# Kernel tuning notes

Hardware: AMD Instinct MI355X
Metric: run time of the kernel (lower is better)

## Reference

```python
import jax, jax.numpy as jnp
import numpy as np
from jax import lax

N_G, E_G, E_LG = 100000, 400000, 1200000
N_T, E_T, E_LGT = 50000, 100000, 300000
D_F, D_MSG_G = 64, 128
VOCAB, D_EMB, D_MSG_T = 780, 128, 128
N_ITERS_G, N_ITERS_T = 4, 4
SCALE = 0.05  # keep relu/sum chains numerically tame over iterations


def setup_inputs() -> dict:
    key = jax.random.key(0)
    ks = jax.random.split(key, 32)
    f32 = jnp.float32
    w = lambda k, sh: jax.random.normal(k, sh, f32) * SCALE
    return {
        "G_f": jax.random.normal(ks[0], (N_G, D_F), f32),
        "G_ef": jax.random.normal(ks[1], (E_G, D_F), f32),
        "G_src": jax.random.randint(ks[2], (E_G,), 0, N_G, jnp.int32),
        "G_dst": jax.random.randint(ks[3], (E_G,), 0, N_G, jnp.int32),
        "G_lg_src": jax.random.randint(ks[4], (E_LG,), 0, E_G, jnp.int32),
        "G_lg_dst": jax.random.randint(ks[5], (E_LG,), 0, E_G, jnp.int32),
        "T_id": jax.random.randint(ks[6], (N_T,), 0, VOCAB, jnp.int32),
        "T_src": jax.random.randint(ks[7], (E_T,), 0, N_T, jnp.int32),
        "T_dst": jax.random.randint(ks[8], (E_T,), 0, N_T, jnp.int32),
        "T_lg_src": jax.random.randint(ks[9], (E_LGT,), 0, E_T, jnp.int32),
        "T_lg_dst": jax.random.randint(ks[10], (E_LGT,), 0, E_T, jnp.int32),
        "embeddings": jax.random.normal(ks[11], (VOCAB, D_EMB), f32),
        "W1": w(ks[12], (D_F, D_MSG_G)),
        "W2": w(ks[13], (D_F, D_MSG_G)),
        "W3": w(ks[14], (D_MSG_G, D_MSG_G)),
        "U1_G": w(ks[15], (D_F, D_MSG_G)),
        "U2_G": w(ks[16], (D_MSG_G, D_MSG_G)),
        "Wz": w(ks[17], (D_EMB, D_MSG_T)),
        "Uz": w(ks[18], (D_MSG_T, D_MSG_T)),
        "Wr": w(ks[19], (D_EMB, D_MSG_T)),
        "Ur": w(ks[20], (D_MSG_T, D_MSG_T)),
        "Wh": w(ks[21], (D_EMB, D_MSG_T)),
        "Uh": w(ks[22], (D_MSG_T, D_MSG_T)),
        "U1_T": w(ks[23], (D_EMB, D_MSG_T)),
        "U2_T": w(ks[24], (D_MSG_T, D_MSG_T)),
    }


def reference(G_f, G_ef, G_src, G_dst, G_lg_src, G_lg_dst,
              T_id, T_src, T_dst, T_lg_src, T_lg_dst,
              embeddings, W1, W2, W3, U1_G, U2_G,
              Wz, Uz, Wr, Ur, Wh, Uh, U1_T, U2_T):
    seg = jax.ops.segment_sum

    # ---- molecule graph G: loopy-BP MLP messages on the line graph ----
    f_src_G = G_f[G_src]                               # [E_G, D_F] copy_src
    base_G = f_src_G @ W1 + G_ef @ W2                  # loop-invariant part of g1_G

    def stepG(msg, _):
        sum_msg = seg(msg[G_lg_src], G_lg_dst, num_segments=E_G)
        return jax.nn.relu(base_G + sum_msg @ W3), None

    msgG0 = jnp.zeros((E_G, D_MSG_G), G_f.dtype)
    msgG, _ = lax.scan(stepG, msgG0, None, length=N_ITERS_G)

    # readout g2_G: sum edge msgs into dst nodes
    sG = seg(msgG, G_dst, num_segments=N_G)
    x_G = jax.nn.relu(G_f @ U1_G + sG @ U2_G)          # [N_G, D_MSG_G]

    # ---- junction tree T: GRU messages on the tree line graph ----
    f_T = embeddings[T_id]                             # one-hot id @ embeddings
    f_src_T = f_T[T_src]                               # [E_T, D_EMB]
    xz, xr, xh = f_src_T @ Wz, f_src_T @ Wr, f_src_T @ Wh

    def stepT(msg, _):
        s = seg(msg[T_lg_src], T_lg_dst, num_segments=E_T)
        z = jax.nn.sigmoid(xz + s @ Uz)
        r = jax.nn.sigmoid(xr + s @ Ur)
        h = jnp.tanh(xh + (r * s) @ Uh)
        return (1.0 - z) * s + z * h, None

    msgT0 = jnp.zeros((E_T, D_MSG_T), f_T.dtype)
    msgT, _ = lax.scan(stepT, msgT0, None, length=N_ITERS_T)

    sT = seg(msgT, T_dst, num_segments=N_T)
    x_T = jax.nn.relu(f_T @ U1_T + sT @ U2_T)          # [N_T, D_MSG_T]

    # concat node readouts (same width) so output is a single array
    return jnp.concatenate([x_G, x_T], axis=0)         # [N_G+N_T, 128]
```

## Files before the change

### kernel.cpp

```cpp
#include <hip/hip_runtime.h>

#define NG 100000
#define EG 400000
#define ELG 1200000
#define NT 50000
#define ET 100000
#define ELGT 300000

#define GEG ((EG + 63) / 64)
#define GET ((ET + 63) / 64)
#define GNG ((NG + 63) / 64)
#define GNT ((NT + 63) / 64)

#define SEG1 EG
#define SEG2 (EG + NG)
#define SEG3 (EG + NG + ET)
#define NSEG_ALL (EG + NG + ET + NT)
#define NE_ALL (ELG + EG + ELGT + ET)

typedef unsigned short u16;
typedef unsigned int u32;
typedef __attribute__((ext_vector_type(8))) short bf16x8;
typedef __attribute__((ext_vector_type(4))) float f32x4;

#define TILE_B 16384

__device__ __forceinline__ float bflo(u32 p){ return __uint_as_float(p << 16); }
__device__ __forceinline__ float bfhi(u32 p){ return __uint_as_float(p & 0xffff0000u); }
__device__ __forceinline__ float bf2f(u16 h){ return __uint_as_float(((u32)h) << 16); }
__device__ __forceinline__ u16 f2bf(float f){
  u32 u = __float_as_uint(f);
  u32 r = u + 0x7fffu + ((u >> 16) & 1u);
  return (u16)(r >> 16);
}
__device__ __forceinline__ float sigm(float x){ return 1.0f / (1.0f + __expf(-x)); }
__device__ __forceinline__ float tanh_(float x){ return 2.0f / (1.0f + __expf(-2.0f * x)) - 1.0f; }
__device__ __forceinline__ float relu_(float x){ return x > 0.0f ? x : 0.0f; }
__device__ __forceinline__ void wfence(){ __builtin_amdgcn_wave_barrier(); }

__device__ __forceinline__ int swz(int r, int c){ return r * 256 + (c ^ ((r & 7) << 4)); }

__device__ __forceinline__ void zero8(float v[8]){
  #pragma unroll
  for (int j = 0; j < 8; j++) v[j] = 0.f;
}
__device__ __forceinline__ uint4 pack8(const float v[8]){
  uint4 o;
  o.x = f2bf(v[0]) | ((u32)f2bf(v[1]) << 16);
  o.y = f2bf(v[2]) | ((u32)f2bf(v[3]) << 16);
  o.z = f2bf(v[4]) | ((u32)f2bf(v[5]) << 16);
  o.w = f2bf(v[6]) | ((u32)f2bf(v[7]) << 16);
  return o;
}
__device__ __forceinline__ uint2 pack4(const f32x4& a){
  uint2 o;
  o.x = (u32)f2bf(a[0]) | ((u32)f2bf(a[1]) << 16);
  o.y = (u32)f2bf(a[2]) | ((u32)f2bf(a[3]) << 16);
  return o;
}
__device__ __forceinline__ uint2 pack4a(const float v[4]){
  uint2 o;
  o.x = (u32)f2bf(v[0]) | ((u32)f2bf(v[1]) << 16);
  o.y = (u32)f2bf(v[2]) | ((u32)f2bf(v[3]) << 16);
  return o;
}
__device__ __forceinline__ void unp4(uint2 u, float v[4]){
  v[0] = bflo(u.x); v[1] = bfhi(u.x); v[2] = bflo(u.y); v[3] = bfhi(u.y);
}
__device__ __forceinline__ bf16x8 packfrag(const float v[8]){
  union { uint4 u; bf16x8 b; } c; c.u = pack8(v); return c.b;
}
__device__ __forceinline__ bf16x8 zfrag(){
  union { uint4 u; bf16x8 b; } c; c.u = make_uint4(0, 0, 0, 0); return c.b;
}
__device__ __forceinline__ bf16x8 as_frag(uint4 u){
  union { uint4 u; bf16x8 b; } c; c.u = u; return c.b;
}

__global__ void k_sniff(const u32* __restrict__ g, int* __restrict__ flag){
  __shared__ int sh[2];
  if (threadIdx.x < 2) sh[threadIdx.x] = 0;
  __syncthreads();
  int c0 = 0, c1 = 0;
  for (int i = 0; i < 16; i++){
    u32 w = g[threadIdx.x * 16 + i];
    u32 lo = w & 0xFFFFu;
    if (lo == 0u) c0++;
    else { u32 e = (lo >> 7) & 0xFFu; if (e >= 96u && e <= 144u) c1++; }
  }
  atomicAdd(&sh[0], c0); atomicAdd(&sh[1], c1);
  __syncthreads();
  if (threadIdx.x == 0) *flag = (sh[0] < 512 && sh[1] > 2048) ? 1 : 0;
}

__global__ void k_cvt_all(const void* p0, const void* p1, const void* p2, const void* p3,
                          const void* p4, const void* p5, const void* p6, const void* p7,
                          const void* p8, const void* p9, const void* p10, const void* p11,
                          const void* p12, float* __restrict__ wm, const int* __restrict__ flagp){
  int i = blockIdx.x * 256 + threadIdx.x;
  if (i >= 188416) return;
  const int offs[14] = {0,8192,16384,32768,40960,57344,73728,90112,106496,122880,139264,155648,172032,188416};
  const void* ps[13] = {p0,p1,p2,p3,p4,p5,p6,p7,p8,p9,p10,p11,p12};
  int w = 0;
  while (i >= offs[w + 1]) w++;
  int li = i - offs[w];
  wm[i] = (*flagp) ? bf2f(((const u16*)ps[w])[li]) : ((const float*)ps[w])[li];
}

__global__ void k_mkfrag_all(const float* __restrict__ wm, u16* __restrict__ frag){
  const int wmo[13] = {0,8192,16384,32768,40960,57344,73728,90112,106496,122880,139264,155648,172032};
  const int nks[13] = {2,2,4,2,4,4,4,4,4,4,4,4,4};
  int b = blockIdx.x;
  int wi = 0, ks = b;
  while (ks >= nks[wi]){ ks -= nks[wi]; wi++; }
  const float* W = wm + wmo[wi];
  int nt = threadIdx.x >> 6, lane = threadIdx.x & 63;
  int kr = ks * 32 + ((lane >> 4) << 3);
  int col = nt * 16 + (lane & 15);
  u16* o = frag + (size_t)b * 4096 + nt * 512 + lane * 8;
  #pragma unroll
  for (int j = 0; j < 8; j++) o[j] = f2bf(W[(size_t)(kr + j) * 128 + col]);
}

__device__ __forceinline__ const void* rowdt(const void* mat, size_t row, int W, int bf){
  return bf ? (const void*)((const u16*)mat + row * (size_t)W)
            : (const void*)((const float*)mat + row * (size_t)W);
}
__device__ __forceinline__ void load8(const void* rowbase, int c8, int bf, float v[8]){
  if (bf){
    uint4 d = ((const uint4*)rowbase)[c8];
    v[0]=bflo(d.x); v[1]=bfhi(d.x); v[2]=bflo(d.y); v[3]=bfhi(d.y);
    v[4]=bflo(d.z); v[5]=bfhi(d.z); v[6]=bflo(d.w); v[7]=bfhi(d.w);
  } else {
    const float4* p = (const float4*)rowbase + (c8 << 1);
    float4 a = p[0], b = p[1];
    v[0]=a.x; v[1]=a.y; v[2]=a.z; v[3]=a.w; v[4]=b.x; v[5]=b.y; v[6]=b.z; v[7]=b.w;
  }
}

__global__ void k_hist_all(const int* __restrict__ Glgd, const int* __restrict__ Gd,
                           const int* __restrict__ Tlgd, const int* __restrict__ Td,
                           int* __restrict__ cnt){
  int e = blockIdx.x * 256 + threadIdx.x;
  if (e >= NE_ALL) return;
  int seg;
  if (e < ELG)                       seg = Glgd[e];
  else if (e < ELG + EG)             seg = SEG1 + Gd[e - ELG];
  else if (e < ELG + EG + ELGT)      seg = SEG2 + Tlgd[e - ELG - EG];
  else                               seg = SEG3 + Td[e - ELG - EG - ELGT];
  atomicAdd(&cnt[seg], 1);
}

__global__ void k_scan1(const int* __restrict__ cnt, int n, int* __restrict__ csum){
  int base = blockIdx.x * 4096, tid = threadIdx.x;
  int s = 0;
  for (int i = 0; i < 16; i++){ int idx = base + i * 256 + tid; if (idx < n) s += cnt[idx]; }
  __shared__ int red[4];
  for (int off = 32; off; off >>= 1) s += __shfl_down(s, off, 64);
  if ((tid & 63) == 0) red[tid >> 6] = s;
  __syncthreads();
  if (tid == 0) csum[blockIdx.x] = red[0] + red[1] + red[2] + red[3];
}

__global__ void k_scan2(int* csum, int nch, int* rowptr, int n){
  if (threadIdx.x == 0){
    int run = 0;
    for (int c = 0; c < nch; c++){ int t = csum[c]; csum[c] = run; run += t; }
    rowptr[n] = run;
  }
}

__global__ void k_scan3(const int* __restrict__ cnt, int n, const int* __restrict__ csum,
                        int* __restrict__ rowptr){
  __shared__ int buf[4096];
  __shared__ int tsum[256];
  int base = blockIdx.x * 4096, tid = threadIdx.x;
  for (int i = 0; i < 16; i++){ int idx = base + i * 256 + tid; buf[i * 256 + tid] = (idx < n) ? cnt[idx] : 0; }
  __syncthreads();
  int run = 0;
  for (int i = 0; i < 16; i++){ int v = buf[tid * 16 + i]; buf[tid * 16 + i] = run; run += v; }
  tsum[tid] = run;
  __syncthreads();
  for (int off = 1; off < 256; off <<= 1){
    int v = (tid >= off) ? tsum[tid - off] : 0;
    __syncthreads();
    tsum[tid] += v;
    __syncthreads();
  }
  int texcl = tsum[tid] - run;
  int cbase = csum[blockIdx.x];
  for (int i = 0; i < 16; i++){
    int idx = base + tid * 16 + i;
    if (idx < n) rowptr[idx] = cbase + texcl + buf[tid * 16 + i];
  }
}

__global__ void k_fill_all(const int* __restrict__ Glgd, const int* __restrict__ Glgs,
                           const int* __restrict__ Gd,
                           const int* __restrict__ Tlgd, const int* __restrict__ Tlgs,
                           const int* __restrict__ Td,
                           const int* __restrict__ rowptr, int* __restrict__ fill,
                           int* __restrict__ col){
  int e = blockIdx.x * 256 + threadIdx.x;
  if (e >= NE_ALL) return;
  int seg, srcv;
  if (e < ELG){                      seg = Glgd[e];                           srcv = Glgs[e]; }
  else if (e < ELG + EG){            int l = e - ELG;                         seg = SEG1 + Gd[l];   srcv = l; }
  else if (e < ELG + EG + ELGT){     int l = e - ELG - EG;                    seg = SEG2 + Tlgd[l]; srcv = Tlgs[l]; }
  else {                             int l = e - ELG - EG - ELGT;             seg = SEG3 + Td[l];   srcv = l; }
  int pos = atomicAdd(&fill[seg], 1);
  col[rowptr[seg] + pos] = srcv;
}


__device__ __forceinline__ void acc8_add(float (&a)[8], uint4 d){
  a[0] += bflo(d.x); a[1] += bfhi(d.x);
  a[2] += bflo(d.y); a[3] += bfhi(d.y);
  a[4] += bflo(d.z); a[5] += bfhi(d.z);
  a[6] += bflo(d.w); a[7] += bfhi(d.w);
}

__device__ __forceinline__ void gather_accum(const int* __restrict__ rowptr,
    const int* __restrict__ colidx, const u16* __restrict__ msg,
    int row, int M, int kg, float (&acc)[4][8])
{
  #pragma unroll
  for (int ks = 0; ks < 4; ks++) zero8(acc[ks]);
  if (row >= M) return;
  int p = rowptr[row], pe = rowptr[row + 1];
  for (; p + 1 < pe; p += 2){
    const uint4* b0 = (const uint4*)(msg + (size_t)colidx[p] * 128);
    const uint4* b1 = (const uint4*)(msg + (size_t)colidx[p + 1] * 128);
    uint4 v0[4], v1[4];
    #pragma unroll
    for (int ks = 0; ks < 4; ks++){ v0[ks] = b0[ks * 4 + kg]; v1[ks] = b1[ks * 4 + kg]; }
    #pragma unroll
    for (int ks = 0; ks < 4; ks++){ acc8_add(acc[ks], v0[ks]); acc8_add(acc[ks], v1[ks]); }
  }
  if (p < pe){
    const uint4* b0 = (const uint4*)(msg + (size_t)colidx[p] * 128);
    #pragma unroll
    for (int ks = 0; ks < 4; ks++){ uint4 v = b0[ks * 4 + kg]; acc8_add(acc[ks], v); }
  }
}

template<int KS>
__device__ __forceinline__ void mma_f(const bf16x8* a, const u16* __restrict__ frag,
                                      f32x4 (&acc)[8])
{
  int lane = threadIdx.x & 63;
  #pragma unroll
  for (int ks = 0; ks < KS; ks++){
    const u16* fb = frag + (size_t)ks * 4096 + lane * 8;
    #pragma unroll
    for (int nt = 0; nt < 8; nt++){
      bf16x8 b = *(const bf16x8*)(fb + (size_t)nt * 512);
      acc[nt] = __builtin_amdgcn_mfma_f32_16x16x32_bf16(a[ks], b, acc[nt], 0, 0, 0);
    }
  }
}

#define INIT_ACC(A) { _Pragma("unroll") for (int n_=0;n_<8;n_++){ A[n_][0]=0.f; A[n_][1]=0.f; A[n_][2]=0.f; A[n_][3]=0.f; } }

__device__ __forceinline__ void repack_store(const char* __restrict__ tile,
    u16* __restrict__ dst, int row0, int M)
{
  int rl = threadIdx.x >> 2, q = threadIdx.x & 3;
  int grow = row0 + rl;
  if (grow < M){
    #pragma unroll
    for (int v = 0; v < 4; v++){
      uint4 d = *(const uint4*)(tile + swz(rl, (v * 4 + q) * 16));
      *(uint4*)(dst + (size_t)grow * 128 + (size_t)(v * 4 + q) * 8) = d;
    }
  }
}

__device__ __forceinline__ size_t fslot(int blk, int w, int nt){
  return ((((size_t)blk * 4 + w) * 8 + nt) * 64 + (threadIdx.x & 63)) * 4;
}

__device__ __forceinline__ void load_catfrag(const void* __restrict__ Gf,
    const void* __restrict__ Gef, const int* __restrict__ Gsrc,
    int arow, int kg, int bf, bf16x8 (&fC)[4])
{
  if (arow < EG){
    int sr = Gsrc[arow];
    const void* ra = rowdt(Gf, (size_t)sr, 64, bf);
    const void* rb = rowdt(Gef, (size_t)arow, 64, bf);
    float t[8];
    load8(ra, kg, bf, t);     fC[0] = packfrag(t);
    load8(ra, 4 + kg, bf, t); fC[1] = packfrag(t);
    load8(rb, kg, bf, t);     fC[2] = packfrag(t);
    load8(rb, 4 + kg, bf, t); fC[3] = packfrag(t);
  } else {
    #pragma unroll
    for (int ks = 0; ks < 4; ks++) fC[ks] = zfrag();
  }
}


__global__ __launch_bounds__(256) void k_init(
    const void* __restrict__ Gf, const void* __restrict__ Gef, const int* __restrict__ Gsrc,
    const u16* __restrict__ fWcat, const int* __restrict__ flagp, u16* __restrict__ msgG,
    const void* __restrict__ emb, const int* __restrict__ Tid, const int* __restrict__ Tsrc,
    const u16* __restrict__ fWz, const u16* __restrict__ fWr, const u16* __restrict__ fWh,
    u16* __restrict__ xzf, u16* __restrict__ xrf, u16* __restrict__ xhf, u16* __restrict__ msgT)
{
  __shared__ char t0[TILE_B];
  int bf = *flagp;
  int lane = threadIdx.x & 63, w = threadIdx.x >> 6;
  int stripe = w * 16, kg = lane >> 4, m16 = lane & 15;
  if (blockIdx.x < GET){
    int blk = blockIdx.x, row0 = blk * 64, arow = row0 + stripe + m16;
    bf16x8 fE[4];
    if (arow < ET){
      int id = Tid[Tsrc[arow]];
      const void* rb = rowdt(emb, (size_t)id, 128, bf);
      #pragma unroll
      for (int ks = 0; ks < 4; ks++){
        float t[8]; load8(rb, ks * 4 + kg, bf, t); fE[ks] = packfrag(t);
      }
    } else {
      #pragma unroll
      for (int ks = 0; ks < 4; ks++) fE[ks] = zfrag();
    }
    f32x4 aZ[8], aR[8]; INIT_ACC(aZ); INIT_ACC(aR);
    mma_f<4>(fE, fWz, aZ);
    mma_f<4>(fE, fWr, aR);
    #pragma unroll
    for (int nt = 0; nt < 8; nt++){
      *(uint2*)(xzf + fslot(blk, w, nt)) = pack4(aZ[nt]);
      *(uint2*)(xrf + fslot(blk, w, nt)) = pack4(aR[nt]);
    }
    f32x4 aH[8]; INIT_ACC(aH);
    mma_f<4>(fE, fWh, aH);
    #pragma unroll
    for (int nt = 0; nt < 8; nt++){
      *(uint2*)(xhf + fslot(blk, w, nt)) = pack4(aH[nt]);
      #pragma unroll
      for (int r = 0; r < 4; r++){
        int rt = stripe + (kg << 2) + r;
        int cb = nt * 32 + m16 * 2;
        *(u16*)(t0 + swz(rt, cb)) = f2bf(sigm(aZ[nt][r]) * tanh_(aH[nt][r]));
      }
    }
    wfence();
    repack_store(t0, msgT, row0, ET);
  } else {
    int blk = blockIdx.x - GET, row0 = blk * 64, arow = row0 + stripe + m16;
    bf16x8 fC[4];
    load_catfrag(Gf, Gef, Gsrc, arow, kg, bf, fC);
    f32x4 acc[8]; INIT_ACC(acc);
    mma_f<4>(fC, fWcat, acc);
    #pragma unroll
    for (int nt = 0; nt < 8; nt++)
      #pragma unroll
      for (int r = 0; r < 4; r++){
        int rt = stripe + (kg << 2) + r;
        int cb = nt * 32 + m16 * 2;
        *(u16*)(t0 + swz(rt, cb)) = f2bf(relu_(acc[nt][r]));
      }
    wfence();
    repack_store(t0, msgG, row0, EG);
  }
}

__global__ __launch_bounds__(256) void k_iter(
    const u16* __restrict__ msgInG, u16* __restrict__ msgOutG,
    const void* __restrict__ Gf, const void* __restrict__ Gef, const int* __restrict__ Gsrc,
    const int* __restrict__ rp, const int* __restrict__ col,
    const u16* __restrict__ fWcat, const u16* __restrict__ fW3, const int* __restrict__ flagp,
    const u16* __restrict__ msgInT, u16* __restrict__ msgOutT,
    const u16* __restrict__ fUz, const u16* __restrict__ fUr, const u16* __restrict__ fUh,
    const u16* __restrict__ xzf, const u16* __restrict__ xrf, const u16* __restrict__ xhf)
{
  __shared__ char t0[TILE_B];
  int lane = threadIdx.x & 63, w = threadIdx.x >> 6;
  int stripe = w * 16, kg = lane >> 4, m16 = lane & 15;
  if (blockIdx.x < GET){
    int blk = blockIdx.x, row0 = blk * 64, arow = row0 + stripe + m16;
    float ga[4][8];
    gather_accum(rp + SEG2, col, msgInT, arow, ET, kg, ga);
    bf16x8 fS[4];
    #pragma unroll
    for (int ks = 0; ks < 4; ks++){
      uint4 pk = pack8(ga[ks]);
      *(uint4*)(t0 + swz(stripe + m16, ks * 64 + kg * 16)) = pk;
      fS[ks] = as_frag(pk);
    }
    f32x4 aZ[8], aR[8]; INIT_ACC(aZ); INIT_ACC(aR);
    mma_f<4>(fS, fUz, aZ);
    mma_f<4>(fS, fUr, aR);
    wfence();
    uint2 zpk[8], wpk[8];
    #pragma unroll
    for (int nt = 0; nt < 8; nt++){
      uint2 z4 = *(const uint2*)(xzf + fslot(blk, w, nt));
      uint2 r4 = *(const uint2*)(xrf + fslot(blk, w, nt));
      float xzv[4], xrv[4], zv[4], wv[4];
      unp4(z4, xzv); unp4(r4, xrv);
      #pragma unroll
      for (int r = 0; r < 4; r++){
        int rt = stripe + (kg << 2) + r;
        int cb = nt * 32 + m16 * 2;
        float s = bf2f(*(const u16*)(t0 + swz(rt, cb)));
        float z = sigm(xzv[r] + aZ[nt][r]);
        float rr = sigm(xrv[r] + aR[nt][r]);
        zv[r] = z;
        wv[r] = s * (1.f - z);
        *(u16*)(t0 + swz(rt, cb)) = f2bf(rr * s);
      }
      zpk[nt] = pack4a(zv); wpk[nt] = pack4a(wv);
    }
    wfence();
    bf16x8 fRS[4];
    #pragma unroll
    for (int ks = 0; ks < 4; ks++)
      fRS[ks] = *(const bf16x8*)(t0 + swz(stripe + m16, ks * 64 + kg * 16));
    f32x4 aH[8]; INIT_ACC(aH);
    mma_f<4>(fRS, fUh, aH);
    wfence();
    #pragma unroll
    for (int nt = 0; nt < 8; nt++){
      uint2 h4 = *(const uint2*)(xhf + fslot(blk, w, nt));
      float xhv[4], zv[4], wv[4];
      unp4(h4, xhv); unp4(zpk[nt], zv); unp4(wpk[nt], wv);
      #pragma unroll
      for (int r = 0; r < 4; r++){
        float h = tanh_(xhv[r] + aH[nt][r]);
        float m = wv[r] + zv[r] * h;
        int rt = stripe + (kg << 2) + r;
        int cb = nt * 32 + m16 * 2;
        *(u16*)(t0 + swz(rt, cb)) = f2bf(m);
      }
    }
    wfence();
    repack_store(t0, msgOutT, row0, ET);
  } else {
    int bf = *flagp;
    int blk = blockIdx.x - GET, row0 = blk * 64, arow = row0 + stripe + m16;
    bf16x8 fC[4];
    load_catfrag(Gf, Gef, Gsrc, arow, kg, bf, fC);
    float ga[4][8];
    gather_accum(rp, col, msgInG, arow, EG, kg, ga);
    bf16x8 fS[4];
    #pragma unroll
    for (int ks = 0; ks < 4; ks++) fS[ks] = packfrag(ga[ks]);
    f32x4 acc[8]; INIT_ACC(acc);
    mma_f<4>(fS, fW3, acc);
    mma_f<4>(fC, fWcat, acc);
    #pragma unroll
    for (int nt = 0; nt < 8; nt++)
      #pragma unroll
      for (int r = 0; r < 4; r++){
        int rt = stripe + (kg << 2) + r;
        int cb = nt * 32 + m16 * 2;
        *(u16*)(t0 + swz(rt, cb)) = f2bf(relu_(acc[nt][r]));
      }
    wfence();
    repack_store(t0, msgOutG, row0, EG);
  }
}

__global__ __launch_bounds__(256) void k_readout(
    const void* __restrict__ Gf, const u16* __restrict__ msgG,
    const int* __restrict__ rp, const int* __restrict__ col,
    const u16* __restrict__ fU1G, const u16* __restrict__ fU2G,
    const void* __restrict__ emb, const int* __restrict__ Tid, const u16* __restrict__ msgT,
    const u16* __restrict__ fU1T, const u16* __restrict__ fU2T,
    const int* __restrict__ flagp, float* __restrict__ out)
{
  int bf = *flagp;
  int lane = threadIdx.x & 63, w = threadIdx.x >> 6;
  int stripe = w * 16, kg = lane >> 4, m16 = lane & 15;
  if (blockIdx.x < GNT){
    int row0 = blockIdx.x * 64, arow = row0 + stripe + m16;
    bf16x8 fE[4];
    if (arow < NT){
      int id = Tid[arow];
      const void* rb = rowdt(emb, (size_t)id, 128, bf);
      #pragma unroll
      for (int ks = 0; ks < 4; ks++){
        float t[8]; load8(rb, ks * 4 + kg, bf, t); fE[ks] = packfrag(t);
      }
    } else {
      #pragma unroll
      for (int ks = 0; ks < 4; ks++) fE[ks] = zfrag();
    }
    float ga[4][8];
    gather_accum(rp + SEG3, col, msgT, arow, NT, kg, ga);
    bf16x8 fS[4];
    #pragma unroll
    for (int ks = 0; ks < 4; ks++) fS[ks] = packfrag(ga[ks]);
    f32x4 acc[8]; INIT_ACC(acc);
    mma_f<4>(fE, fU1T, acc);
    mma_f<4>(fS, fU2T, acc);
    #pragma unroll
    for (int nt = 0; nt < 8; nt++)
      #pragma unroll
      for (int r = 0; r < 4; r++){
        int R = row0 + stripe + (kg << 2) + r;
        if (R < NT) out[(size_t)(NG + R) * 128 + nt * 16 + m16] = relu_(acc[nt][r]);
      }
  } else {
    int row0 = (blockIdx.x - GNT) * 64, arow = row0 + stripe + m16;
    bf16x8 fG[2];
    if (arow < NG){
      const void* ra = rowdt(Gf, (size_t)arow, 64, bf);
      float t[8];
      load8(ra, kg, bf, t);     fG[0] = packfrag(t);
      load8(ra, 4 + kg, bf, t); fG[1] = packfrag(t);
    } else { fG[0] = zfrag(); fG[1] = zfrag(); }
    float ga[4][8];
    gather_accum(rp + SEG1, col, msgG, arow, NG, kg, ga);
    bf16x8 fS[4];
    #pragma unroll
    for (int ks = 0; ks < 4; ks++) fS[ks] = packfrag(ga[ks]);
    f32x4 acc[8]; INIT_ACC(acc);
    mma_f<2>(fG, fU1G, acc);
    mma_f<4>(fS, fU2G, acc);
    #pragma unroll
    for (int nt = 0; nt < 8; nt++)
      #pragma unroll
      for (int r = 0; r < 4; r++){
        int R = row0 + stripe + (kg << 2) + r;
        if (R < NG) out[(size_t)R * 128 + nt * 16 + m16] = relu_(acc[nt][r]);
      }
  }
}

extern "C" void kernel_launch(void* const* d_in, const int* in_sizes, int n_in,
                              void* d_out, int out_size, void* d_ws, size_t ws_size,
                              hipStream_t stream)
{
  const void* G_f      = d_in[0];
  const void* G_ef     = d_in[1];
  const int*  G_src    = (const int*)d_in[2];
  const int*  G_dst    = (const int*)d_in[3];
  const int*  G_lg_src = (const int*)d_in[4];
  const int*  G_lg_dst = (const int*)d_in[5];
  const int*  T_id     = (const int*)d_in[6];
  const int*  T_src    = (const int*)d_in[7];
  const int*  T_dst    = (const int*)d_in[8];
  const int*  T_lg_src = (const int*)d_in[9];
  const int*  T_lg_dst = (const int*)d_in[10];
  const void* emb      = d_in[11];
  float* out = (float*)d_out;
  (void)in_sizes; (void)n_in; (void)out_size; (void)ws_size;

  size_t off = 0;
  auto alloc = [&](size_t bytes) -> char* {
    char* p = (char*)d_ws + off;
    off += (bytes + 255) & ~(size_t)255;
    return p;
  };

  int*   flag = (int*)alloc(256);
  float* wm   = (float*)alloc(sizeof(float) * 188416);
  u16*   frag = (u16*)alloc(2 * 46 * 4096);
  const u16* fWcat = frag;
  const u16* fW3   = frag + (size_t)4  * 4096;
  const u16* fU1G  = frag + (size_t)8  * 4096;
  const u16* fU2G  = frag + (size_t)10 * 4096;
  const u16* fWz   = frag + (size_t)14 * 4096;
  const u16* fUz   = frag + (size_t)18 * 4096;
  const u16* fWr   = frag + (size_t)22 * 4096;
  const u16* fUr   = frag + (size_t)26 * 4096;
  const u16* fWh   = frag + (size_t)30 * 4096;
  const u16* fUh   = frag + (size_t)34 * 4096;
  const u16* fU1T  = frag + (size_t)38 * 4096;
  const u16* fU2T  = frag + (size_t)42 * 4096;

  int* rp   = (int*)alloc(sizeof(int) * (NSEG_ALL + 1));
  int* col  = (int*)alloc(sizeof(int) * NE_ALL);
  int* cnt  = (int*)alloc(sizeof(int) * 2 * NSEG_ALL);
  int* csum = (int*)alloc(sizeof(int) * 256);
  u16* msgGA = (u16*)alloc((size_t)EG * 128 * 2);
  u16* msgGB = (u16*)alloc((size_t)EG * 128 * 2);
  u16* xzf   = (u16*)alloc((size_t)GET * 8192 * 2);
  u16* xrf   = (u16*)alloc((size_t)GET * 8192 * 2);
  u16* xhf   = (u16*)alloc((size_t)GET * 8192 * 2);
  u16* msgTA = (u16*)alloc((size_t)ET * 128 * 2);
  u16* msgTB = (u16*)alloc((size_t)ET * 128 * 2);

  k_sniff<<<1, 256, 0, stream>>>((const u32*)G_ef, flag);
  k_cvt_all<<<(188416 + 255) / 256, 256, 0, stream>>>(
      d_in[12], d_in[13], d_in[14], d_in[15], d_in[16], d_in[17], d_in[18],
      d_in[19], d_in[20], d_in[21], d_in[22], d_in[23], d_in[24], wm, flag);
  k_mkfrag_all<<<46, 512, 0, stream>>>(wm, frag);

  hipMemsetAsync(cnt, 0, sizeof(int) * 2 * NSEG_ALL, stream);
  k_hist_all<<<(NE_ALL + 255) / 256, 256, 0, stream>>>(G_lg_dst, G_dst, T_lg_dst, T_dst, cnt);
  int nch = (NSEG_ALL + 4095) / 4096;
  k_scan1<<<nch, 256, 0, stream>>>(cnt, NSEG_ALL, csum);
  k_scan2<<<1, 64, 0, stream>>>(csum, nch, rp, NSEG_ALL);
  k_scan3<<<nch, 256, 0, stream>>>(cnt, NSEG_ALL, csum, rp);
  k_fill_all<<<(NE_ALL + 255) / 256, 256, 0, stream>>>(
      G_lg_dst, G_lg_src, G_dst, T_lg_dst, T_lg_src, T_dst, rp, cnt + NSEG_ALL, col);

  k_init<<<GET + GEG, 256, 0, stream>>>(G_f, G_ef, G_src, fWcat, flag, msgGA,
                                        emb, T_id, T_src, fWz, fWr, fWh, xzf, xrf, xhf, msgTA);
  k_iter<<<GET + GEG, 256, 0, stream>>>(msgGA, msgGB, G_f, G_ef, G_src, rp, col, fWcat, fW3, flag,
                                        msgTA, msgTB, fUz, fUr, fUh, xzf, xrf, xhf);
  k_iter<<<GET + GEG, 256, 0, stream>>>(msgGB, msgGA, G_f, G_ef, G_src, rp, col, fWcat, fW3, flag,
                                        msgTB, msgTA, fUz, fUr, fUh, xzf, xrf, xhf);
  k_iter<<<GET + GEG, 256, 0, stream>>>(msgGA, msgGB, G_f, G_ef, G_src, rp, col, fWcat, fW3, flag,
                                        msgTA, msgTB, fUz, fUr, fUh, xzf, xrf, xhf);
  k_readout<<<GNT + GNG, 256, 0, stream>>>(G_f, msgGB, rp, col, fU1G, fU2G,
                                           emb, T_id, msgTB, fU1T, fU2T, flag, out);
}
```

Before: 1.246 ms.

## Pad CSR rows to multiples of four and cut register pressure in GRU kernels

CSR rows are padded to multiples of four and filled with a dummy index that points at an extra zeroed message row, so the gather loop always loads four neighbour rows per step with no tail branch. The GRU step is reordered to compute r, then h, then z, using a second LDS tile so fewer accumulator arrays are live at once. k_init, k_iter and k_readout get launch bounds that request higher occupancy, and in the G branch of k_iter and in k_readout the gathers are moved ahead of the other loads. This trades extra padded loads of a zero row and added LDS use for more memory-level parallelism and occupancy; the tighter register limit may cause spills.

```diff
diff --git a/kernel.cpp b/kernel.cpp
--- a/kernel.cpp
+++ b/kernel.cpp
@@ -17,6 +17,7 @@
 #define SEG3 (EG + NG + ET)
 #define NSEG_ALL (EG + NG + ET + NT)
 #define NE_ALL (ELG + EG + ELGT + ET)
+#define NE_PAD (NE_ALL + 3 * NSEG_ALL + 64)
 
 typedef unsigned short u16;
 typedef unsigned int u32;
@@ -56,12 +57,6 @@
   uint2 o;
   o.x = (u32)f2bf(a[0]) | ((u32)f2bf(a[1]) << 16);
   o.y = (u32)f2bf(a[2]) | ((u32)f2bf(a[3]) << 16);
-  return o;
-}
-__device__ __forceinline__ uint2 pack4a(const float v[4]){
-  uint2 o;
-  o.x = (u32)f2bf(v[0]) | ((u32)f2bf(v[1]) << 16);
-  o.y = (u32)f2bf(v[2]) | ((u32)f2bf(v[3]) << 16);
   return o;
 }
 __device__ __forceinline__ void unp4(uint2 u, float v[4]){
@@ -154,7 +149,10 @@
 __global__ void k_scan1(const int* __restrict__ cnt, int n, int* __restrict__ csum){
   int base = blockIdx.x * 4096, tid = threadIdx.x;
   int s = 0;
-  for (int i = 0; i < 16; i++){ int idx = base + i * 256 + tid; if (idx < n) s += cnt[idx]; }
+  for (int i = 0; i < 16; i++){
+    int idx = base + i * 256 + tid;
+    if (idx < n) s += (cnt[idx] + 3) & ~3;
+  }
   __shared__ int red[4];
   for (int off = 32; off; off >>= 1) s += __shfl_down(s, off, 64);
   if ((tid & 63) == 0) red[tid >> 6] = s;
@@ -175,7 +173,10 @@
   __shared__ int buf[4096];
   __shared__ int tsum[256];
   int base = blockIdx.x * 4096, tid = threadIdx.x;
-  for (int i = 0; i < 16; i++){ int idx = base + i * 256 + tid; buf[i * 256 + tid] = (idx < n) ? cnt[idx] : 0; }
+  for (int i = 0; i < 16; i++){
+    int idx = base + i * 256 + tid;
+    buf[i * 256 + tid] = (idx < n) ? ((cnt[idx] + 3) & ~3) : 0;
+  }
   __syncthreads();
   int run = 0;
   for (int i = 0; i < 16; i++){ int v = buf[tid * 16 + i]; buf[tid * 16 + i] = run; run += v; }
@@ -212,6 +213,24 @@
   col[rowptr[seg] + pos] = srcv;
 }
 
+__global__ void k_fill_pad(const int* __restrict__ cnt, const int* __restrict__ rowptr,
+                           int* __restrict__ col){
+  int seg = blockIdx.x * 256 + threadIdx.x;
+  if (seg >= NSEG_ALL) return;
+  int dummy = (seg < SEG2) ? EG : ET;
+  int start = rowptr[seg] + cnt[seg];
+  int end = rowptr[seg + 1];
+  for (int q = start; q < end; q++) col[q] = dummy;
+}
+
+__global__ void k_zero_dummy(u16* a, u16* b, u16* c, u16* d){
+  int i = threadIdx.x;
+  if (i < 128){
+    a[(size_t)EG * 128 + i] = 0; b[(size_t)EG * 128 + i] = 0;
+    c[(size_t)ET * 128 + i] = 0; d[(size_t)ET * 128 + i] = 0;
+  }
+}
+
 
 __device__ __forceinline__ void acc8_add(float (&a)[8], uint4 d){
   a[0] += bflo(d.x); a[1] += bfhi(d.x);
@@ -228,19 +247,23 @@
   for (int ks = 0; ks < 4; ks++) zero8(acc[ks]);
   if (row >= M) return;
   int p = rowptr[row], pe = rowptr[row + 1];
-  for (; p + 1 < pe; p += 2){
-    const uint4* b0 = (const uint4*)(msg + (size_t)colidx[p] * 128);
-    const uint4* b1 = (const uint4*)(msg + (size_t)colidx[p + 1] * 128);
-    uint4 v0[4], v1[4];
-    #pragma unroll
-    for (int ks = 0; ks < 4; ks++){ v0[ks] = b0[ks * 4 + kg]; v1[ks] = b1[ks * 4 + kg]; }
-    #pragma unroll
-    for (int ks = 0; ks < 4; ks++){ acc8_add(acc[ks], v0[ks]); acc8_add(acc[ks], v1[ks]); }
-  }
-  if (p < pe){
-    const uint4* b0 = (const uint4*)(msg + (size_t)colidx[p] * 128);
-    #pragma unroll
-    for (int ks = 0; ks < 4; ks++){ uint4 v = b0[ks * 4 + kg]; acc8_add(acc[ks], v); }
+  for (; p < pe; p += 4){
+    int i0 = colidx[p], i1 = colidx[p + 1], i2 = colidx[p + 2], i3 = colidx[p + 3];
+    const uint4* b0 = (const uint4*)(msg + (size_t)i0 * 128);
+    const uint4* b1 = (const uint4*)(msg + (size_t)i1 * 128);
+    const uint4* b2 = (const uint4*)(msg + (size_t)i2 * 128);
+    const uint4* b3 = (const uint4*)(msg + (size_t)i3 * 128);
+    uint4 v0[4], v1[4], v2[4], v3[4];
+    #pragma unroll
+    for (int ks = 0; ks < 4; ks++){
+      v0[ks] = b0[ks * 4 + kg]; v1[ks] = b1[ks * 4 + kg];
+      v2[ks] = b2[ks * 4 + kg]; v3[ks] = b3[ks * 4 + kg];
+    }
+    #pragma unroll
+    for (int ks = 0; ks < 4; ks++){
+      acc8_add(acc[ks], v0[ks]); acc8_add(acc[ks], v1[ks]);
+      acc8_add(acc[ks], v2[ks]); acc8_add(acc[ks], v3[ks]);
+    }
   }
 }
 
@@ -300,7 +323,7 @@
 }
 
 
-__global__ __launch_bounds__(256) void k_init(
+__global__ __launch_bounds__(256, 4) void k_init(
     const void* __restrict__ Gf, const void* __restrict__ Gef, const int* __restrict__ Gsrc,
     const u16* __restrict__ fWcat, const int* __restrict__ flagp, u16* __restrict__ msgG,
     const void* __restrict__ emb, const int* __restrict__ Tid, const int* __restrict__ Tsrc,
@@ -325,24 +348,31 @@
       #pragma unroll
       for (int ks = 0; ks < 4; ks++) fE[ks] = zfrag();
     }
-    f32x4 aZ[8], aR[8]; INIT_ACC(aZ); INIT_ACC(aR);
-    mma_f<4>(fE, fWz, aZ);
-    mma_f<4>(fE, fWr, aR);
+    f32x4 acc[8];
+    uint2 zpk[8];
+    INIT_ACC(acc);
+    mma_f<4>(fE, fWz, acc);
     #pragma unroll
     for (int nt = 0; nt < 8; nt++){
-      *(uint2*)(xzf + fslot(blk, w, nt)) = pack4(aZ[nt]);
-      *(uint2*)(xrf + fslot(blk, w, nt)) = pack4(aR[nt]);
-    }
-    f32x4 aH[8]; INIT_ACC(aH);
-    mma_f<4>(fE, fWh, aH);
+      zpk[nt] = pack4(acc[nt]);
+      *(uint2*)(xzf + fslot(blk, w, nt)) = zpk[nt];
+    }
+    INIT_ACC(acc);
+    mma_f<4>(fE, fWr, acc);
+    #pragma unroll
+    for (int nt = 0; nt < 8; nt++)
+      *(uint2*)(xrf + fslot(blk, w, nt)) = pack4(acc[nt]);
+    INIT_ACC(acc);
+    mma_f<4>(fE, fWh, acc);
     #pragma unroll
     for (int nt = 0; nt < 8; nt++){
-      *(uint2*)(xhf + fslot(blk, w, nt)) = pack4(aH[nt]);
+      *(uint2*)(xhf + fslot(blk, w, nt)) = pack4(acc[nt]);
+      float xzv[4]; unp4(zpk[nt], xzv);
       #pragma unroll
       for (int r = 0; r < 4; r++){
         int rt = stripe + (kg << 2) + r;
         int cb = nt * 32 + m16 * 2;
-        *(u16*)(t0 + swz(rt, cb)) = f2bf(sigm(aZ[nt][r]) * tanh_(aH[nt][r]));
+        *(u16*)(t0 + swz(rt, cb)) = f2bf(sigm(xzv[r]) * tanh_(acc[nt][r]));
       }
     }
     wfence();
@@ -366,7 +396,7 @@
   }
 }
 
-__global__ __launch_bounds__(256) void k_iter(
+__global__ __launch_bounds__(256, 4) void k_iter(
     const u16* __restrict__ msgInG, u16* __restrict__ msgOutG,
     const void* __restrict__ Gf, const void* __restrict__ Gef, const int* __restrict__ Gsrc,
     const int* __restrict__ rp, const int* __restrict__ col,
@@ -376,6 +406,7 @@
     const u16* __restrict__ xzf, const u16* __restrict__ xrf, const u16* __restrict__ xhf)
 {
   __shared__ char t0[TILE_B];
+  __shared__ char t1[TILE_B];
   int lane = threadIdx.x & 63, w = threadIdx.x >> 6;
   int stripe = w * 16, kg = lane >> 4, m16 = lane & 15;
   if (blockIdx.x < GET){
@@ -389,50 +420,62 @@
       *(uint4*)(t0 + swz(stripe + m16, ks * 64 + kg * 16)) = pk;
       fS[ks] = as_frag(pk);
     }
-    f32x4 aZ[8], aR[8]; INIT_ACC(aZ); INIT_ACC(aR);
-    mma_f<4>(fS, fUz, aZ);
-    mma_f<4>(fS, fUr, aR);
-    wfence();
-    uint2 zpk[8], wpk[8];
+    f32x4 acc[8];
+    INIT_ACC(acc);
+    mma_f<4>(fS, fUr, acc);
+    wfence();
     #pragma unroll
     for (int nt = 0; nt < 8; nt++){
-      uint2 z4 = *(const uint2*)(xzf + fslot(blk, w, nt));
       uint2 r4 = *(const uint2*)(xrf + fslot(blk, w, nt));
-      float xzv[4], xrv[4], zv[4], wv[4];
-      unp4(z4, xzv); unp4(r4, xrv);
+      float xrv[4]; unp4(r4, xrv);
       #pragma unroll
       for (int r = 0; r < 4; r++){
         int rt = stripe + (kg << 2) + r;
         int cb = nt * 32 + m16 * 2;
         float s = bf2f(*(const u16*)(t0 + swz(rt, cb)));
-        float z = sigm(xzv[r] + aZ[nt][r]);
-        float rr = sigm(xrv[r] + aR[nt][r]);
-        zv[r] = z;
-        wv[r] = s * (1.f - z);
-        *(u16*)(t0 + swz(rt, cb)) = f2bf(rr * s);
-      }
-      zpk[nt] = pack4a(zv); wpk[nt] = pack4a(wv);
+        float rr = sigm(xrv[r] + acc[nt][r]);
+        *(u16*)(t1 + swz(rt, cb)) = f2bf(rr * s);
+      }
     }
     wfence();
     bf16x8 fRS[4];
     #pragma unroll
     for (int ks = 0; ks < 4; ks++)
-      fRS[ks] = *(const bf16x8*)(t0 + swz(stripe + m16, ks * 64 + kg * 16));
-    f32x4 aH[8]; INIT_ACC(aH);
-    mma_f<4>(fRS, fUh, aH);
+      fRS[ks] = *(const bf16x8*)(t1 + swz(stripe + m16, ks * 64 + kg * 16));
+    INIT_ACC(acc);
+    mma_f<4>(fRS, fUh, acc);
     wfence();
     #pragma unroll
     for (int nt = 0; nt < 8; nt++){
       uint2 h4 = *(const uint2*)(xhf + fslot(blk, w, nt));
-      float xhv[4], zv[4], wv[4];
-      unp4(h4, xhv); unp4(zpk[nt], zv); unp4(wpk[nt], wv);
-      #pragma unroll
-      for (int r = 0; r < 4; r++){
-        float h = tanh_(xhv[r] + aH[nt][r]);
-        float m = wv[r] + zv[r] * h;
+      float xhv[4]; unp4(h4, xhv);
+      #pragma unroll
+      for (int r = 0; r < 4; r++){
         int rt = stripe + (kg << 2) + r;
         int cb = nt * 32 + m16 * 2;
-        *(u16*)(t0 + swz(rt, cb)) = f2bf(m);
+        *(u16*)(t1 + swz(rt, cb)) = f2bf(tanh_(xhv[r] + acc[nt][r]));
+      }
+    }
+    wfence();
+    bf16x8 fS2[4];
+    #pragma unroll
+    for (int ks = 0; ks < 4; ks++)
+      fS2[ks] = *(const bf16x8*)(t0 + swz(stripe + m16, ks * 64 + kg * 16));
+    INIT_ACC(acc);
+    mma_f<4>(fS2, fUz, acc);
+    wfence();
+    #pragma unroll
+    for (int nt = 0; nt < 8; nt++){
+      uint2 z4 = *(const uint2*)(xzf + fslot(blk, w, nt));
+      float xzv[4]; unp4(z4, xzv);
+      #pragma unroll
+      for (int r = 0; r < 4; r++){
+        int rt = stripe + (kg << 2) + r;
+        int cb = nt * 32 + m16 * 2;
+        float z = sigm(xzv[r] + acc[nt][r]);
+        float s = bf2f(*(const u16*)(t0 + swz(rt, cb)));
+        float h = bf2f(*(const u16*)(t1 + swz(rt, cb)));
+        *(u16*)(t0 + swz(rt, cb)) = f2bf((1.f - z) * s + z * h);
       }
     }
     wfence();
@@ -440,13 +483,13 @@
   } else {
     int bf = *flagp;
     int blk = blockIdx.x - GET, row0 = blk * 64, arow = row0 + stripe + m16;
-    bf16x8 fC[4];
-    load_catfrag(Gf, Gef, Gsrc, arow, kg, bf, fC);
     float ga[4][8];
     gather_accum(rp, col, msgInG, arow, EG, kg, ga);
     bf16x8 fS[4];
     #pragma unroll
     for (int ks = 0; ks < 4; ks++) fS[ks] = packfrag(ga[ks]);
+    bf16x8 fC[4];
+    load_catfrag(Gf, Gef, Gsrc, arow, kg, bf, fC);
     f32x4 acc[8]; INIT_ACC(acc);
     mma_f<4>(fS, fW3, acc);
     mma_f<4>(fC, fWcat, acc);
@@ -463,7 +506,7 @@
   }
 }
 
-__global__ __launch_bounds__(256) void k_readout(
+__global__ __launch_bounds__(256, 4) void k_readout(
     const void* __restrict__ Gf, const u16* __restrict__ msgG,
     const int* __restrict__ rp, const int* __restrict__ col,
     const u16* __restrict__ fU1G, const u16* __restrict__ fU2G,
@@ -476,6 +519,11 @@
   int stripe = w * 16, kg = lane >> 4, m16 = lane & 15;
   if (blockIdx.x < GNT){
     int row0 = blockIdx.x * 64, arow = row0 + stripe + m16;
+    float ga[4][8];
+    gather_accum(rp + SEG3, col, msgT, arow, NT, kg, ga);
+    bf16x8 fS[4];
+    #pragma unroll
+    for (int ks = 0; ks < 4; ks++) fS[ks] = packfrag(ga[ks]);
     bf16x8 fE[4];
     if (arow < NT){
       int id = Tid[arow];
@@ -488,14 +536,9 @@
       #pragma unroll
       for (int ks = 0; ks < 4; ks++) fE[ks] = zfrag();
     }
-    float ga[4][8];
-    gather_accum(rp + SEG3, col, msgT, arow, NT, kg, ga);
-    bf16x8 fS[4];
-    #pragma unroll
-    for (int ks = 0; ks < 4; ks++) fS[ks] = packfrag(ga[ks]);
     f32x4 acc[8]; INIT_ACC(acc);
+    mma_f<4>(fS, fU2T, acc);
     mma_f<4>(fE, fU1T, acc);
-    mma_f<4>(fS, fU2T, acc);
     #pragma unroll
     for (int nt = 0; nt < 8; nt++)
       #pragma unroll
@@ -505,6 +548,11 @@
       }
   } else {
     int row0 = (blockIdx.x - GNT) * 64, arow = row0 + stripe + m16;
+    float ga[4][8];
+    gather_accum(rp + SEG1, col, msgG, arow, NG, kg, ga);
+    bf16x8 fS[4];
+    #pragma unroll
+    for (int ks = 0; ks < 4; ks++) fS[ks] = packfrag(ga[ks]);
     bf16x8 fG[2];
     if (arow < NG){
       const void* ra = rowdt(Gf, (size_t)arow, 64, bf);
@@ -512,14 +560,9 @@
       load8(ra, kg, bf, t);     fG[0] = packfrag(t);
       load8(ra, 4 + kg, bf, t); fG[1] = packfrag(t);
     } else { fG[0] = zfrag(); fG[1] = zfrag(); }
-    float ga[4][8];
-    gather_accum(rp + SEG1, col, msgG, arow, NG, kg, ga);
-    bf16x8 fS[4];
-    #pragma unroll
-    for (int ks = 0; ks < 4; ks++) fS[ks] = packfrag(ga[ks]);
     f32x4 acc[8]; INIT_ACC(acc);
+    mma_f<4>(fS, fU2G, acc);
     mma_f<2>(fG, fU1G, acc);
-    mma_f<4>(fS, fU2G, acc);
     #pragma unroll
     for (int nt = 0; nt < 8; nt++)
       #pragma unroll
@@ -573,22 +616,23 @@
   const u16* fU2T  = frag + (size_t)42 * 4096;
 
   int* rp   = (int*)alloc(sizeof(int) * (NSEG_ALL + 1));
-  int* col  = (int*)alloc(sizeof(int) * NE_ALL);
+  int* col  = (int*)alloc(sizeof(int) * NE_PAD);
   int* cnt  = (int*)alloc(sizeof(int) * 2 * NSEG_ALL);
   int* csum = (int*)alloc(sizeof(int) * 256);
-  u16* msgGA = (u16*)alloc((size_t)EG * 128 * 2);
-  u16* msgGB = (u16*)alloc((size_t)EG * 128 * 2);
+  u16* msgGA = (u16*)alloc((size_t)(EG + 1) * 128 * 2);
+  u16* msgGB = (u16*)alloc((size_t)(EG + 1) * 128 * 2);
   u16* xzf   = (u16*)alloc((size_t)GET * 8192 * 2);
   u16* xrf   = (u16*)alloc((size_t)GET * 8192 * 2);
   u16* xhf   = (u16*)alloc((size_t)GET * 8192 * 2);
-  u16* msgTA = (u16*)alloc((size_t)ET * 128 * 2);
-  u16* msgTB = (u16*)alloc((size_t)ET * 128 * 2);
+  u16* msgTA = (u16*)alloc((size_t)(ET + 1) * 128 * 2);
+  u16* msgTB = (u16*)alloc((size_t)(ET + 1) * 128 * 2);
 
   k_sniff<<<1, 256, 0, stream>>>((const u32*)G_ef, flag);
   k_cvt_all<<<(188416 + 255) / 256, 256, 0, stream>>>(
       d_in[12], d_in[13], d_in[14], d_in[15], d_in[16], d_in[17], d_in[18],
       d_in[19], d_in[20], d_in[21], d_in[22], d_in[23], d_in[24], wm, flag);
   k_mkfrag_all<<<46, 512, 0, stream>>>(wm, frag);
+  k_zero_dummy<<<1, 128, 0, stream>>>(msgGA, msgGB, msgTA, msgTB);
 
   hipMemsetAsync(cnt, 0, sizeof(int) * 2 * NSEG_ALL, stream);
   k_hist_all<<<(NE_ALL + 255) / 256, 256, 0, stream>>>(G_lg_dst, G_dst, T_lg_dst, T_dst, cnt);
@@ -598,6 +642,7 @@
   k_scan3<<<nch, 256, 0, stream>>>(cnt, NSEG_ALL, csum, rp);
   k_fill_all<<<(NE_ALL + 255) / 256, 256, 0, stream>>>(
       G_lg_dst, G_lg_src, G_dst, T_lg_dst, T_lg_src, T_dst, rp, cnt + NSEG_ALL, col);
+  k_fill_pad<<<(NSEG_ALL + 255) / 256, 256, 0, stream>>>(cnt, rp, col);
 
   k_init<<<GET + GEG, 256, 0, stream>>>(G_f, G_ef, G_src, fWcat, flag, msgGA,
                                         emb, T_id, T_src, fWz, fWr, fWh, xzf, xrf, xhf, msgTA);
```

Measured after the change: 1.098 ms. 11.9% less time.
